# Kernel optimization log

Hardware: AMD Instinct MI355X
Metric: run time of the kernel (lower is better)

## Reference

```python
import jax, jax.numpy as jnp
import numpy as np

N_IN = 1024      # input dim, also acts as the loop/sequence length (u_input.shape[2])
N_HIDDEN = 128   # state dim H
BATCH = 2


def setup_inputs() -> dict:
    key = jax.random.key(0)
    k1, k2, k3, k4 = jax.random.split(key, 4)
    u_input = jax.random.normal(k1, (BATCH, N_IN, N_IN, 1), jnp.float32)
    delta = jnp.asarray(0.01, jnp.float32)  # ZOH step size
    # HiPPO-like eigenvalues: real part -1/2, spread imaginary parts
    lambda_re = jnp.full((N_HIDDEN,), -0.5, jnp.float32)
    lambda_im = jax.random.normal(k2, (N_HIDDEN,), jnp.float32) * jnp.float32(N_HIDDEN / 4)
    std = jnp.float32((1.0 / N_IN) ** 0.5)
    b_re = jax.random.normal(k3, (N_HIDDEN, N_IN), jnp.float32) * std
    b_im = jax.random.normal(k4, (N_HIDDEN, N_IN), jnp.float32) * std
    return {"u_input": u_input, "delta": delta, "lambda_re": lambda_re,
            "lambda_im": lambda_im, "b_re": b_re, "b_im": b_im}


def reference(u_input, delta, lambda_re, lambda_im, b_re, b_im):
    # Complex continuous-time parameters (complex64; original used complex128)
    lam = (lambda_re + 1j * lambda_im).astype(jnp.complex64)      # (H,)
    b_mat = (b_re + 1j * b_im).astype(jnp.complex64)              # (H, n_in)
    # ZOH discretization
    lambda_bar = jnp.exp(lam * delta)                             # (H,)
    b_bar = ((lambda_bar - 1.0) / lam)[:, None] * b_mat           # (H, n_in)
    # Loop length in original is u_input.shape[2] (= n_in), indexing dim 1
    T = u_input.shape[2]
    u_seq = u_input[:, :T, :, 0].astype(jnp.complex64)            # (B, T, n_in)
    bu = jnp.einsum('hi,bti->tbh', b_bar, u_seq)                  # (T, B, H)
    B = u_input.shape[0]
    H = lam.shape[0]
    # Faithful to the original broadcasting quirk: lambda_bar (H,) * x (B,H,1)
    # broadcasts the state to (B, H, H) from step 1 onward.
    x0 = jnp.zeros((B, H, H), jnp.complex64)

    def step(x, bu_t):
        x = lambda_bar[None, None, :] * x + bu_t[:, :, None]      # (B, H, H)
        return x, x

    _, out = jax.lax.scan(step, x0, bu)                           # (T, B, H, H)
    return out
```

## Files before the change

kernel.cpp:

```cpp
#include <hip/hip_runtime.h>
#include <math.h>

#define T_LEN   1024
#define N_INPUT 1024
#define H_DIM   128
#define BATCH   2
#define TC      128
#define NC      8

#define PLANE   ((size_t)T_LEN * BATCH * H_DIM * H_DIM)
#define TSTRIDE ((size_t)BATCH * H_DIM * H_DIM)


__global__ __launch_bounds__(1024)
void bu_kernel(const float* __restrict__ u,
               const float* __restrict__ delta_p,
               const float* __restrict__ lre,
               const float* __restrict__ lim,
               const float* __restrict__ b_re,
               const float* __restrict__ b_im,
               float* __restrict__ out) {
    __shared__ float su[8][N_INPUT];
    __shared__ float sred[2048];

    int blk = blockIdx.x;
    int b   = blk >> 7;
    int tg  = blk & 127;
    int tid = threadIdx.x;
    int j   = tid >> 3;
    int c8  = tid & 7;

    const float4* g4 = (const float4*)(u + ((size_t)b * T_LEN + (size_t)tg * 8) * N_INPUT);
    float4* s4 = (float4*)su;
    s4[tid]        = g4[tid];
    s4[tid + 1024] = g4[tid + 1024];
    __syncthreads();

    const float4* br4 = (const float4*)b_re;
    const float4* bi4 = (const float4*)b_im;
    int bbase = j * 256 + c8;

    float accr[8], acci[8];
#pragma unroll
    for (int t = 0; t < 8; ++t) { accr[t] = 0.0f; acci[t] = 0.0f; }

    for (int ii = 0; ii < 32; ++ii) {
        float4 br = br4[bbase + ii * 8];
        float4 bi = bi4[bbase + ii * 8];
        int w = (ii * 8 + c8) * 4;
#pragma unroll
        for (int t = 0; t < 8; ++t) {
            float4 uv = *(const float4*)&su[t][w];
            accr[t] += br.x * uv.x + br.y * uv.y + br.z * uv.z + br.w * uv.w;
            acci[t] += bi.x * uv.x + bi.y * uv.y + bi.z * uv.z + bi.w * uv.w;
        }
    }

    float delta = delta_p[0];
    float ar = lre[j], ai = lim[j];
    float e = expf(ar * delta);
    float s_, co;
    sincosf(ai * delta, &s_, &co);
    float lbr = e * co, lbi = e * s_;
    float nr = lbr - 1.0f, ni = lbi, dd = ar * ar + ai * ai;
    float cr = (nr * ar + ni * ai) / dd, ci = (ni * ar - nr * ai) / dd;

#pragma unroll
    for (int t = 0; t < 8; ++t) {
        float r = accr[t], i = acci[t];
        r += __shfl_xor(r, 1);  i += __shfl_xor(i, 1);
        r += __shfl_xor(r, 2);  i += __shfl_xor(i, 2);
        r += __shfl_xor(r, 4);  i += __shfl_xor(i, 4);
        if (c8 == 0) {
            sred[j * 16 + t * 2]     = cr * r - ci * i;
            sred[j * 16 + t * 2 + 1] = cr * i + ci * r;
        }
    }
    __syncthreads();

    size_t wb = (size_t)(1008 + (tg >> 3)) * TSTRIDE + (size_t)b * 16384 + (size_t)(tg & 7) * 16;
#pragma unroll
    for (int r = 0; r < 2; ++r) {
        int e2 = tid + r * 1024;
        out[wb + (size_t)(e2 >> 4) * 128 + (e2 & 15)] = sred[e2];
    }
}

__global__ __launch_bounds__(1024)
void scan_kernel(const float* __restrict__ delta_p,
                 const float* __restrict__ lre,
                 const float* __restrict__ lim,
                 float* out) {
    __shared__ float2 sbu[T_LEN];
    __shared__ float2 sP[NC][H_DIM];
    __shared__ float2 sX[NC][H_DIM];

    int blk = blockIdx.x;
    int b   = blk >> 7;
    int j   = blk & 127;
    int tid = threadIdx.x;
    int k   = tid & 127;
    int c   = tid >> 7;

    {
        int s = tid >> 6, w = tid & 63;
        const float* p = out + (size_t)(1008 + s) * TSTRIDE + (size_t)b * 16384
                             + (size_t)j * 128 + (size_t)w * 2;
        sbu[s * 64 + w] = *(const float2*)p;
    }

    float delta = delta_p[0];
    float ar = lre[k], ai = lim[k];
    float e = expf(ar * delta);
    float s_, co;
    sincosf(ai * delta, &s_, &co);
    float lbr = e * co, lbi = e * s_;
    __syncthreads();

    {
        float pr = 0.0f, pi = 0.0f;
        int t0 = c * TC;
        for (int s2 = 0; s2 < TC; ++s2) {
            float2 bu = sbu[t0 + s2];
            float nr2 = lbr * pr - lbi * pi + bu.x;
            float ni2 = lbr * pi + lbi * pr + bu.y;
            pr = nr2; pi = ni2;
        }
        sP[c][k] = make_float2(pr, pi);
    }
    __syncthreads();

    if (tid < H_DIM) {
        float gr = lbr, gi = lbi;
#pragma unroll
        for (int q = 0; q < 7; ++q) {
            float tr = gr * gr - gi * gi;
            float ti = 2.0f * gr * gi;
            gr = tr; gi = ti;
        }
        float xr = 0.0f, xi = 0.0f;
#pragma unroll
        for (int cc = 0; cc < NC; ++cc) {
            sX[cc][tid] = make_float2(xr, xi);
            float2 p = sP[cc][tid];
            float nr2 = gr * xr - gi * xi + p.x;
            float ni2 = gr * xi + gi * xr + p.y;
            xr = nr2; xi = ni2;
        }
    }
    __syncthreads();

    {
        float2 x0 = sX[c][k];
        float xr = x0.x, xi = x0.y;
        int t0 = c * TC;
        float* outr = out + ((size_t)b * H_DIM + j) * H_DIM + k + (size_t)t0 * TSTRIDE;
        for (int s2 = 0; s2 < TC; ++s2) {
            float2 bu = sbu[t0 + s2];
            float nr2 = lbr * xr - lbi * xi + bu.x;
            float ni2 = lbr * xi + lbi * xr + bu.y;
            xr = nr2; xi = ni2;
            __builtin_nontemporal_store(xr, outr + (size_t)s2 * TSTRIDE);
        }
    }
}

extern "C" void kernel_launch(void* const* d_in, const int* in_sizes, int n_in,
                              void* d_out, int out_size, void* d_ws, size_t ws_size,
                              hipStream_t stream) {
    const float* u      = (const float*)d_in[0];
    const float* delta  = (const float*)d_in[1];
    const float* lre    = (const float*)d_in[2];
    const float* lim    = (const float*)d_in[3];
    const float* b_re   = (const float*)d_in[4];
    const float* b_im   = (const float*)d_in[5];
    float* out = (float*)d_out;

    if ((size_t)out_size >= PLANE) {
        bu_kernel<<<BATCH * 128, 1024, 0, stream>>>(u, delta, lre, lim, b_re, b_im, out);
        scan_kernel<<<BATCH * H_DIM, 1024, 0, stream>>>(delta, lre, lim, out);
    }
}
```

Before: 200.4 us.

## Vectorize scan stores to 16 bytes and split time into more chunks

```diff
diff --git a/kernel.cpp b/kernel.cpp
--- a/kernel.cpp
+++ b/kernel.cpp
@@ -5,11 +5,13 @@
 #define N_INPUT 1024
 #define H_DIM   128
 #define BATCH   2
-#define TC      128
-#define NC      8
+#define TC      32
+#define NC      32
 
 #define PLANE   ((size_t)T_LEN * BATCH * H_DIM * H_DIM)
 #define TSTRIDE ((size_t)BATCH * H_DIM * H_DIM)
+
+typedef float vfloat4 __attribute__((ext_vector_type(4)));
 
 
 __global__ __launch_bounds__(1024)
@@ -20,15 +22,17 @@
                const float* __restrict__ b_re,
                const float* __restrict__ b_im,
                float* __restrict__ out) {
-    __shared__ float su[8][N_INPUT];
+    __shared__ __align__(16) float su[8][N_INPUT];
     __shared__ float sred[2048];
 
     int blk = blockIdx.x;
     int b   = blk >> 7;
     int tg  = blk & 127;
     int tid = threadIdx.x;
-    int j   = tid >> 3;
-    int c8  = tid & 7;
+    int j2  = tid >> 4;
+    int c16 = tid & 15;
+    int jA  = j2;
+    int jB  = j2 + 64;
 
     const float4* g4 = (const float4*)(u + ((size_t)b * T_LEN + (size_t)tg * 8) * N_INPUT);
     float4* s4 = (float4*)su;
@@ -38,42 +42,63 @@
 
     const float4* br4 = (const float4*)b_re;
     const float4* bi4 = (const float4*)b_im;
-    int bbase = j * 256 + c8;
-
-    float accr[8], acci[8];
-#pragma unroll
-    for (int t = 0; t < 8; ++t) { accr[t] = 0.0f; acci[t] = 0.0f; }
-
-    for (int ii = 0; ii < 32; ++ii) {
-        float4 br = br4[bbase + ii * 8];
-        float4 bi = bi4[bbase + ii * 8];
-        int w = (ii * 8 + c8) * 4;
+    int baseA = jA * 256 + c16;
+    int baseB = jB * 256 + c16;
+
+    float arA[8], aiA[8], arB[8], aiB[8];
+#pragma unroll
+    for (int t = 0; t < 8; ++t) { arA[t] = 0.f; aiA[t] = 0.f; arB[t] = 0.f; aiB[t] = 0.f; }
+
+    for (int ii = 0; ii < 16; ++ii) {
+        float4 brA = br4[baseA + ii * 16];
+        float4 biA = bi4[baseA + ii * 16];
+        float4 brB = br4[baseB + ii * 16];
+        float4 biB = bi4[baseB + ii * 16];
+        int w = (ii * 16 + c16) * 4;
 #pragma unroll
         for (int t = 0; t < 8; ++t) {
             float4 uv = *(const float4*)&su[t][w];
-            accr[t] += br.x * uv.x + br.y * uv.y + br.z * uv.z + br.w * uv.w;
-            acci[t] += bi.x * uv.x + bi.y * uv.y + bi.z * uv.z + bi.w * uv.w;
+            arA[t] += brA.x * uv.x + brA.y * uv.y + brA.z * uv.z + brA.w * uv.w;
+            aiA[t] += biA.x * uv.x + biA.y * uv.y + biA.z * uv.z + biA.w * uv.w;
+            arB[t] += brB.x * uv.x + brB.y * uv.y + brB.z * uv.z + brB.w * uv.w;
+            aiB[t] += biB.x * uv.x + biB.y * uv.y + biB.z * uv.z + biB.w * uv.w;
         }
     }
 
     float delta = delta_p[0];
-    float ar = lre[j], ai = lim[j];
-    float e = expf(ar * delta);
-    float s_, co;
-    sincosf(ai * delta, &s_, &co);
-    float lbr = e * co, lbi = e * s_;
-    float nr = lbr - 1.0f, ni = lbi, dd = ar * ar + ai * ai;
-    float cr = (nr * ar + ni * ai) / dd, ci = (ni * ar - nr * ai) / dd;
+    float crA, ciA, crB, ciB;
+    {
+        float ar = lre[jA], ai = lim[jA];
+        float e = expf(ar * delta);
+        float s_, co;
+        sincosf(ai * delta, &s_, &co);
+        float nr = e * co - 1.0f, ni = e * s_, dd = ar * ar + ai * ai;
+        crA = (nr * ar + ni * ai) / dd;
+        ciA = (ni * ar - nr * ai) / dd;
+    }
+    {
+        float ar = lre[jB], ai = lim[jB];
+        float e = expf(ar * delta);
+        float s_, co;
+        sincosf(ai * delta, &s_, &co);
+        float nr = e * co - 1.0f, ni = e * s_, dd = ar * ar + ai * ai;
+        crB = (nr * ar + ni * ai) / dd;
+        ciB = (ni * ar - nr * ai) / dd;
+    }
 
 #pragma unroll
     for (int t = 0; t < 8; ++t) {
-        float r = accr[t], i = acci[t];
-        r += __shfl_xor(r, 1);  i += __shfl_xor(i, 1);
-        r += __shfl_xor(r, 2);  i += __shfl_xor(i, 2);
-        r += __shfl_xor(r, 4);  i += __shfl_xor(i, 4);
-        if (c8 == 0) {
-            sred[j * 16 + t * 2]     = cr * r - ci * i;
-            sred[j * 16 + t * 2 + 1] = cr * i + ci * r;
+        float rA = arA[t], iA = aiA[t], rB = arB[t], iB = aiB[t];
+#pragma unroll
+        for (int m = 1; m <= 8; m <<= 1) {
+            rA += __shfl_xor(rA, m);  iA += __shfl_xor(iA, m);
+            rB += __shfl_xor(rB, m);  iB += __shfl_xor(iB, m);
+        }
+        if (c16 == 0) {
+            sred[jA * 16 + t * 2]     = crA * rA - ciA * iA;
+            sred[jA * 16 + t * 2 + 1] = crA * iA + ciA * rA;
+            sred[jB * 16 + t * 2]     = crB * rB - ciB * iB;
+            sred[jB * 16 + t * 2 + 1] = crB * iB + ciB * rB;
         }
     }
     __syncthreads();
@@ -91,7 +116,7 @@
                  const float* __restrict__ lre,
                  const float* __restrict__ lim,
                  float* out) {
-    __shared__ float2 sbu[T_LEN];
+    __shared__ __align__(16) float2 sbu[T_LEN];
     __shared__ float2 sP[NC][H_DIM];
     __shared__ float2 sX[NC][H_DIM];
 
@@ -99,8 +124,9 @@
     int b   = blk >> 7;
     int j   = blk & 127;
     int tid = threadIdx.x;
-    int k   = tid & 127;
-    int c   = tid >> 7;
+    int kg  = tid & 31;
+    int c   = tid >> 5;
+    int k0  = kg * 4;
 
     {
         int s = tid >> 6, w = tid & 63;
@@ -110,30 +136,53 @@
     }
 
     float delta = delta_p[0];
-    float ar = lre[k], ai = lim[k];
-    float e = expf(ar * delta);
-    float s_, co;
-    sincosf(ai * delta, &s_, &co);
-    float lbr = e * co, lbi = e * s_;
-    __syncthreads();
-
-    {
-        float pr = 0.0f, pi = 0.0f;
+    float lbr[4], lbi[4];
+#pragma unroll
+    for (int q = 0; q < 4; ++q) {
+        float ar = lre[k0 + q], ai = lim[k0 + q];
+        float e = expf(ar * delta);
+        float s_, co;
+        sincosf(ai * delta, &s_, &co);
+        lbr[q] = e * co;
+        lbi[q] = e * s_;
+    }
+    __syncthreads();
+
+    const float4* sbu4 = (const float4*)sbu;
+
+    {
+        float pr[4] = {0.f, 0.f, 0.f, 0.f}, pi[4] = {0.f, 0.f, 0.f, 0.f};
         int t0 = c * TC;
-        for (int s2 = 0; s2 < TC; ++s2) {
-            float2 bu = sbu[t0 + s2];
-            float nr2 = lbr * pr - lbi * pi + bu.x;
-            float ni2 = lbr * pi + lbi * pr + bu.y;
-            pr = nr2; pi = ni2;
-        }
-        sP[c][k] = make_float2(pr, pi);
+#pragma unroll 4
+        for (int s2 = 0; s2 < TC; s2 += 2) {
+            float4 bb = sbu4[(t0 + s2) >> 1];
+#pragma unroll
+            for (int q = 0; q < 4; ++q) {
+                float nr = lbr[q] * pr[q] - lbi[q] * pi[q] + bb.x;
+                float ni = lbr[q] * pi[q] + lbi[q] * pr[q] + bb.y;
+                pr[q] = nr; pi[q] = ni;
+            }
+#pragma unroll
+            for (int q = 0; q < 4; ++q) {
+                float nr = lbr[q] * pr[q] - lbi[q] * pi[q] + bb.z;
+                float ni = lbr[q] * pi[q] + lbi[q] * pr[q] + bb.w;
+                pr[q] = nr; pi[q] = ni;
+            }
+        }
+#pragma unroll
+        for (int q = 0; q < 4; ++q) sP[c][k0 + q] = make_float2(pr[q], pi[q]);
     }
     __syncthreads();
 
     if (tid < H_DIM) {
-        float gr = lbr, gi = lbi;
-#pragma unroll
-        for (int q = 0; q < 7; ++q) {
+        int k = tid;
+        float ar = lre[k], ai = lim[k];
+        float e = expf(ar * delta);
+        float s_, co;
+        sincosf(ai * delta, &s_, &co);
+        float gr = e * co, gi = e * s_;
+#pragma unroll
+        for (int q = 0; q < 5; ++q) {
             float tr = gr * gr - gi * gi;
             float ti = 2.0f * gr * gi;
             gr = tr; gi = ti;
@@ -141,26 +190,44 @@
         float xr = 0.0f, xi = 0.0f;
 #pragma unroll
         for (int cc = 0; cc < NC; ++cc) {
-            sX[cc][tid] = make_float2(xr, xi);
-            float2 p = sP[cc][tid];
-            float nr2 = gr * xr - gi * xi + p.x;
-            float ni2 = gr * xi + gi * xr + p.y;
-            xr = nr2; xi = ni2;
-        }
-    }
-    __syncthreads();
-
-    {
-        float2 x0 = sX[c][k];
-        float xr = x0.x, xi = x0.y;
+            sX[cc][k] = make_float2(xr, xi);
+            float2 p = sP[cc][k];
+            float nr = gr * xr - gi * xi + p.x;
+            float ni = gr * xi + gi * xr + p.y;
+            xr = nr; xi = ni;
+        }
+    }
+    __syncthreads();
+
+    {
+        float xr[4], xi[4];
+#pragma unroll
+        for (int q = 0; q < 4; ++q) {
+            float2 x0 = sX[c][k0 + q];
+            xr[q] = x0.x; xi[q] = x0.y;
+        }
         int t0 = c * TC;
-        float* outr = out + ((size_t)b * H_DIM + j) * H_DIM + k + (size_t)t0 * TSTRIDE;
-        for (int s2 = 0; s2 < TC; ++s2) {
-            float2 bu = sbu[t0 + s2];
-            float nr2 = lbr * xr - lbi * xi + bu.x;
-            float ni2 = lbr * xi + lbi * xr + bu.y;
-            xr = nr2; xi = ni2;
-            __builtin_nontemporal_store(xr, outr + (size_t)s2 * TSTRIDE);
+        float* outp = out + (size_t)t0 * TSTRIDE + (size_t)b * 16384
+                          + (size_t)j * 128 + k0;
+#pragma unroll 4
+        for (int s2 = 0; s2 < TC; s2 += 2) {
+            float4 bb = sbu4[(t0 + s2) >> 1];
+#pragma unroll
+            for (int q = 0; q < 4; ++q) {
+                float nr = lbr[q] * xr[q] - lbi[q] * xi[q] + bb.x;
+                float ni = lbr[q] * xi[q] + lbi[q] * xr[q] + bb.y;
+                xr[q] = nr; xi[q] = ni;
+            }
+            vfloat4 v0 = (vfloat4){xr[0], xr[1], xr[2], xr[3]};
+#pragma unroll
+            for (int q = 0; q < 4; ++q) {
+                float nr = lbr[q] * xr[q] - lbi[q] * xi[q] + bb.z;
+                float ni = lbr[q] * xi[q] + lbi[q] * xr[q] + bb.w;
+                xr[q] = nr; xi[q] = ni;
+            }
+            vfloat4 v1 = (vfloat4){xr[0], xr[1], xr[2], xr[3]};
+            __builtin_nontemporal_store(v0, (vfloat4*)(outp + (size_t)s2 * TSTRIDE));
+            __builtin_nontemporal_store(v1, (vfloat4*)(outp + (size_t)(s2 + 1) * TSTRIDE));
         }
     }
 }
```

Result: slower. 205.9 us (+2.7%).
